# Performance work log

Hardware: AMD Instinct MI355X
Metric: run time of the kernel (lower is better)

Reference implementation:

```python
import jax, jax.numpy as jnp
import numpy as np

EPS = 1e-5
NEG_SLOPE = 0.2  # GATConv default negative_slope


def layer_norm(x, g, b):
    mu = jnp.mean(x, axis=-1, keepdims=True)
    var = jnp.mean((x - mu) ** 2, axis=-1, keepdims=True)
    return (x - mu) * jax.lax.rsqrt(var + EPS) * g + b


def setup_inputs() -> dict:
    key = jax.random.key(0)
    ks = jax.random.split(key, 16)
    B, NPG = 64, 1024          # graphs, fine nodes per graph
    NF = B * NPG               # 65536 fine nodes
    IN, HID, ATT, H, LLM = 1024, 1024, 64, 8, 2048
    D = ATT * H                # 512
    w = lambda k, shp: (jax.random.normal(k, shp, jnp.float32) * 0.02)
    # structured bipartite star edges: fine node i -> global node i // NPG
    edge_index = jnp.stack([jnp.arange(NF, dtype=jnp.int32),
                            (jnp.arange(NF, dtype=jnp.int32) // NPG)])
    return {
        "x_fine": jax.random.normal(ks[0], (NF, IN), jnp.float32),
        "x_global": jax.random.normal(ks[1], (B, D), jnp.float32),
        "edge_index_fine_global": edge_index,
        "nf_g": jnp.ones((IN,), jnp.float32), "nf_b": jnp.zeros((IN,), jnp.float32),
        "ip_w1": w(ks[2], (IN, HID)), "ip_b1": jnp.zeros((HID,), jnp.float32),
        "ip_w2": w(ks[3], (HID, D)), "ip_b2": jnp.zeros((D,), jnp.float32),
        "ng_g": jnp.ones((D,), jnp.float32), "ng_b": jnp.zeros((D,), jnp.float32),
        "gat_ws": w(ks[4], (D, D)), "gat_wd": w(ks[5], (D, D)),
        "att_s": w(ks[6], (1, H, ATT)), "att_d": w(ks[7], (1, H, ATT)),
        "gat_bias": jnp.zeros((D,), jnp.float32),
        "gp_w": w(ks[8], (D, LLM)), "gp_b": jnp.zeros((LLM,), jnp.float32),
        "fp_w": w(ks[9], (D, LLM)), "fp_b": jnp.zeros((LLM,), jnp.float32),
    }


def reference(x_fine, x_global, edge_index_fine_global,
              nf_g, nf_b, ip_w1, ip_b1, ip_w2, ip_b2, ng_g, ng_b,
              gat_ws, gat_wd, att_s, att_d, gat_bias,
              gp_w, gp_b, fp_w, fp_b):
    B = x_global.shape[0]
    H = att_s.shape[1]
    C = x_global.shape[1] // H

    # fine branch: LayerNorm -> MLP projection to H*C
    xf = layer_norm(x_fine, nf_g, nf_b)
    xf = jax.nn.relu(xf @ ip_w1 + ip_b1) @ ip_w2 + ip_b2      # [NF, H*C]
    xg = layer_norm(x_global, ng_g, ng_b)                      # [B, H*C]

    # bipartite GATConv (eval mode: attention dropout disabled)
    xs = (xf @ gat_ws).reshape(-1, H, C)                       # [NF, H, C]
    xd = (xg @ gat_wd).reshape(B, H, C)                        # [B, H, C]
    a_s = jnp.sum(xs * att_s, axis=-1)                         # [NF, H]
    a_d = jnp.sum(xd * att_d, axis=-1)                         # [B, H]

    row, col = edge_index_fine_global[0], edge_index_fine_global[1]
    loops = jnp.arange(B, dtype=row.dtype)                     # add_self_loops: nodes < min(NF,B)
    rows = jnp.concatenate([row, loops])
    cols = jnp.concatenate([col, loops])
    # PyG removes pre-existing self-loop edges; emulate by masking them out
    self_mask = jnp.concatenate([row == col, jnp.zeros((B,), bool)])

    logits = jax.nn.leaky_relu(a_s[rows] + a_d[cols], NEG_SLOPE)   # [E+B, H]
    logits = jnp.where(self_mask[:, None], -jnp.inf, logits)
    m = jax.ops.segment_max(logits, cols, num_segments=B)         # [B, H]
    e = jnp.exp(logits - m[cols])
    e = jnp.where(self_mask[:, None], 0.0, e)
    denom = jax.ops.segment_sum(e, cols, num_segments=B)
    alpha = e / denom[cols]                                       # [E+B, H]

    msg = xs[rows] * alpha[..., None]                              # [E+B, H, C]
    agg = jax.ops.segment_sum(msg, cols, num_segments=B)          # [B, H, C]
    xg = agg.reshape(B, H * C) + gat_bias + xg                    # GAT out + residual

    og = (xg @ gp_w + gp_b)[:, None, :]                            # [B, 1, LLM]
    of = (xf @ fp_w + fp_b).reshape(B, -1, fp_w.shape[1])          # [B, NPG, LLM]
    return jnp.concatenate([og, of], axis=1)                       # [B, 1+NPG, LLM]
```

## Files before the change

### kernel.cpp

```cpp
#include <hip/hip_runtime.h>
#include <hip/hip_bf16.h>
#include <math.h>

typedef __bf16 bf16_t;
typedef bf16_t bf16x8 __attribute__((ext_vector_type(8)));
typedef bf16_t bf16x4 __attribute__((ext_vector_type(4)));
typedef float f32x4 __attribute__((ext_vector_type(4)));

#define DEVINL __device__ __forceinline__

DEVINL float wave_reduce_sum(float v) {
#pragma unroll
  for (int o = 32; o > 0; o >>= 1) v += __shfl_down(v, o);
  return v;
}
DEVINL float block_reduce_sum256(float v, float* red) {
  int tid = threadIdx.x;
  __syncthreads();
  v = wave_reduce_sum(v);
  if ((tid & 63) == 0) red[tid >> 6] = v;
  __syncthreads();
  return red[0] + red[1] + red[2] + red[3];
}

__global__ __launch_bounds__(256) void k_ln_fine(const float* __restrict__ x,
                                                 const float* __restrict__ g,
                                                 const float* __restrict__ b,
                                                 bf16_t* __restrict__ out) {
  constexpr int CPT = 4, COLS = 1024;
  __shared__ float red[8];
  const size_t row = blockIdx.x;
  const float* xr = x + row * COLS;
  const int c0 = threadIdx.x * CPT;
  float v[CPT];
#pragma unroll
  for (int j = 0; j < CPT; j++) v[j] = xr[c0 + j];
  float s = 0;
#pragma unroll
  for (int j = 0; j < CPT; j++) s += v[j];
  const float mu = block_reduce_sum256(s, red) * (1.0f / COLS);
  float q = 0;
#pragma unroll
  for (int j = 0; j < CPT; j++) { float d = v[j] - mu; q += d * d; }
  const float var = block_reduce_sum256(q, red) * (1.0f / COLS);
  const float rs = rsqrtf(var + 1e-5f);
  bf16x4 o;
#pragma unroll
  for (int j = 0; j < CPT; j++)
    o[j] = (bf16_t)((v[j] - mu) * rs * g[c0 + j] + b[c0 + j]);
  *(bf16x4*)(out + row * COLS + c0) = o;
}

__global__ __launch_bounds__(256) void k_prep(
    const float* __restrict__ ip_w1, const float* __restrict__ ip_w2,
    const float* __restrict__ fp_w, const float* __restrict__ gat_wd,
    const float* __restrict__ att_d, const float* __restrict__ gat_ws,
    const float* __restrict__ att_s, const float* __restrict__ x_global,
    const float* __restrict__ ng_g, const float* __restrict__ ng_b,
    bf16_t* __restrict__ w1t, bf16_t* __restrict__ w2t, bf16_t* __restrict__ fpt,
    float* __restrict__ wd_att, float* __restrict__ wsatt, float* __restrict__ xg) {
  __shared__ float t[32][33];
  __shared__ float red[8];
  const int bid = blockIdx.x, tid = threadIdx.x;
  if (bid < 2560) {
    const float* src;
    bf16_t* dst;
    int N, n0, k0;
    if (bid < 1024) {
      src = ip_w1; dst = w1t; N = 1024;
      n0 = (bid & 31) * 32; k0 = (bid >> 5) * 32;
    } else if (bid < 1536) {
      const int rel = bid - 1024;
      src = ip_w2; dst = w2t; N = 512;
      n0 = (rel & 15) * 32; k0 = (rel >> 4) * 32;
    } else {
      const int rel = bid - 1536;
      src = fp_w; dst = fpt; N = 2048;
      n0 = (rel & 63) * 32; k0 = (rel >> 6) * 32;
    }
    const int K = (bid < 1536) ? 1024 : 512;
    const int tx = tid & 31, ty = tid >> 5;
#pragma unroll
    for (int i = 0; i < 32; i += 8)
      t[ty + i][tx] = src[(size_t)(k0 + ty + i) * N + n0 + tx];
    __syncthreads();
#pragma unroll
    for (int i = 0; i < 32; i += 8)
      dst[(size_t)(n0 + ty + i) * K + k0 + tx] = (bf16_t)t[tx][ty + i];
  } else if (bid < 2564) {
    const int rel = bid - 2560;
    const float* W = (rel < 2) ? gat_wd : gat_ws;
    const float* att = (rel < 2) ? att_d : att_s;
    float* outp = (rel < 2) ? wd_att : wsatt;
    const int k = (rel & 1) * 256 + tid;
#pragma unroll
    for (int h = 0; h < 8; h++) {
      float s = 0;
      for (int c = 0; c < 64; c++)
        s += W[(size_t)k * 512 + h * 64 + c] * att[h * 64 + c];
      outp[k * 8 + h] = s;
    }
  } else {
    const int row = bid - 2564;
    const float* xr = x_global + (size_t)row * 512;
    const int c0 = tid * 2;
    float v0 = xr[c0], v1 = xr[c0 + 1];
    const float mu = block_reduce_sum256(v0 + v1, red) * (1.0f / 512);
    const float d0 = v0 - mu, d1 = v1 - mu;
    const float var = block_reduce_sum256(d0 * d0 + d1 * d1, red) * (1.0f / 512);
    const float rs = rsqrtf(var + 1e-5f);
    xg[(size_t)row * 512 + c0] = d0 * rs * ng_g[c0] + ng_b[c0];
    xg[(size_t)row * 512 + c0 + 1] = d1 * rs * ng_g[c0 + 1] + ng_b[c0 + 1];
  }
}

template <int N, int K, int EPI>
__global__ __launch_bounds__(256, 2) void gemm_bt(const bf16_t* __restrict__ A,
                                                  const bf16_t* __restrict__ Bt,
                                                  const float* __restrict__ bias,
                                                  void* __restrict__ Cout) {
  __shared__ bf16_t As[128 * 64];
  __shared__ bf16_t Bs[128 * 64];
  const int tid = threadIdx.x;
  const int lane = tid & 63;
  const int wid = tid >> 6;
  const int wm = wid >> 1, wn = wid & 1;
  const size_t arow0 = (size_t)blockIdx.x * 128;
  const int bcol0 = blockIdx.y * 128;

  f32x4 acc[4][4] = {};
  const int kTiles = K / 64;
  for (int kt = 0; kt < kTiles; ++kt) {
    const int k0 = kt * 64;
#pragma unroll
    for (int i = 0; i < 4; ++i) {
      const int c = i * 256 + tid;
      const int r = c >> 3, kc = (c & 7) * 8;
      const bf16_t* ga = A + (arow0 + r) * K + k0 + kc;
      __builtin_amdgcn_global_load_lds(
          (const __attribute__((address_space(1))) void*)ga,
          (__attribute__((address_space(3))) void*)(As + c * 8), 16, 0, 0);
      const bf16_t* gb = Bt + ((size_t)bcol0 + r) * K + k0 + kc;
      __builtin_amdgcn_global_load_lds(
          (const __attribute__((address_space(1))) void*)gb,
          (__attribute__((address_space(3))) void*)(Bs + c * 8), 16, 0, 0);
    }
    __syncthreads();
#pragma unroll
    for (int kk = 0; kk < 2; ++kk) {
      bf16x8 af[4], bfr[4];
      const int kofs = kk * 32 + (lane >> 4) * 8;
#pragma unroll
      for (int m = 0; m < 4; ++m)
        af[m] = *(const bf16x8*)(As + (wm * 64 + m * 16 + (lane & 15)) * 64 + kofs);
#pragma unroll
      for (int n = 0; n < 4; ++n)
        bfr[n] = *(const bf16x8*)(Bs + (wn * 64 + n * 16 + (lane & 15)) * 64 + kofs);
#pragma unroll
      for (int m = 0; m < 4; ++m)
#pragma unroll
        for (int n = 0; n < 4; ++n)
          acc[m][n] = __builtin_amdgcn_mfma_f32_16x16x32_bf16(af[m], bfr[n], acc[m][n], 0, 0, 0);
    }
    __syncthreads();
  }
  const int lr = (lane >> 4) * 4;
  const int lc = lane & 15;
#pragma unroll
  for (int n = 0; n < 4; ++n) {
    const int col = bcol0 + wn * 64 + n * 16 + lc;
    const float bv = bias[col];
#pragma unroll
    for (int m = 0; m < 4; ++m) {
#pragma unroll
      for (int j = 0; j < 4; ++j) {
        const size_t row = arow0 + wm * 64 + m * 16 + lr + j;
        float v = acc[m][n][j] + bv;
        if constexpr (EPI == 0) v = v > 0.0f ? v : 0.0f;
        if constexpr (EPI == 3) {
          const size_t orow = row + (row >> 10) + 1;
          ((float*)Cout)[orow * (size_t)N + col] = v;
        } else {
          ((bf16_t*)Cout)[row * (size_t)N + col] = (bf16_t)v;
        }
      }
    }
  }
}

__global__ __launch_bounds__(256) void k_as(const bf16_t* __restrict__ xf,
                                            const float* __restrict__ wsatt,
                                            float* __restrict__ a_s) {
  const int tid = threadIdx.x, l = tid & 63, wid = tid >> 6;
  float wreg[64];
#pragma unroll
  for (int q = 0; q < 16; q++) {
    const float4 v = *(const float4*)(wsatt + l * 64 + q * 4);
    wreg[q * 4 + 0] = v.x; wreg[q * 4 + 1] = v.y;
    wreg[q * 4 + 2] = v.z; wreg[q * 4 + 3] = v.w;
  }
  const size_t base = (size_t)blockIdx.x * 128 + wid * 32;
  for (int rr = 0; rr < 32; rr++) {
    const size_t i = base + rr;
    const bf16x8 v = *(const bf16x8*)(xf + i * 512 + l * 8);
    float p[8] = {};
#pragma unroll
    for (int u = 0; u < 8; u++) {
      const float xv = (float)v[u];
#pragma unroll
      for (int h = 0; h < 8; h++) p[h] += xv * wreg[u * 8 + h];
    }
#pragma unroll
    for (int h = 0; h < 8; h++)
#pragma unroll
      for (int mk = 1; mk < 64; mk <<= 1) p[h] += __shfl_xor(p[h], mk);
    float outv = 0.0f;
#pragma unroll
    for (int h = 0; h < 8; h++) outv = (l == h) ? p[h] : outv;
    if (l < 8) a_s[i * 8 + l] = outv;
  }
}

__global__ __launch_bounds__(512) void k_alpha_z(const float* __restrict__ a_s,
                                                 const bf16_t* __restrict__ xf,
                                                 const float* __restrict__ xg,
                                                 const float* __restrict__ wd_att,
                                                 float* __restrict__ zq) {
  __shared__ float sal[8][260];
  const int b = blockIdx.x >> 2, qq = blockIdx.x & 3;
  const int tid = threadIdx.x, l = tid & 63, h = tid >> 6;
  float pa = 0;
#pragma unroll
  for (int u = 0; u < 8; u++)
    pa += xg[b * 512 + l * 8 + u] * wd_att[(l * 8 + u) * 8 + h];
#pragma unroll
  for (int mk = 1; mk < 64; mk <<= 1) pa += __shfl_xor(pa, mk);
  const float ad = pa;
  const float* asb = a_s + (size_t)b * 1024 * 8;
  float lg[16];
  float lmax = -1e30f;
#pragma unroll
  for (int j = 0; j < 16; j++) {
    const float a = asb[(l + j * 64) * 8 + h] + ad;
    lg[j] = a > 0.0f ? a : 0.2f * a;
    lmax = fmaxf(lmax, lg[j]);
  }
  float lself = -INFINITY;
  if (l == 0 && b != 0) {
    const float a = a_s[b * 8 + h] + ad;
    lself = a > 0.0f ? a : 0.2f * a;
  }
  lmax = fmaxf(lmax, lself);
#pragma unroll
  for (int mk = 1; mk < 64; mk <<= 1) lmax = fmaxf(lmax, __shfl_xor(lmax, mk));
  float ps = 0;
#pragma unroll
  for (int j = 0; j < 16; j++) { lg[j] = __expf(lg[j] - lmax); ps += lg[j]; }
  const float eself = (l == 0 && lself != -INFINITY) ? __expf(lself - lmax) : 0.0f;
  ps += eself;
#pragma unroll
  for (int mk = 1; mk < 64; mk <<= 1) ps += __shfl_xor(ps, mk);
  const float inv = 1.0f / ps;
#pragma unroll
  for (int j = 0; j < 4; j++) sal[h][l + j * 64] = lg[qq * 4 + j] * inv;
  if (l == 0) sal[h][256] = (qq == 0) ? eself * inv : 0.0f;
  __syncthreads();
  float zp[8] = {};
  const bf16_t* xb = xf + ((size_t)b * 1024 + qq * 256) * 512 + l * 8;
  for (int i = 0; i < 256; i += 2) {
    const float a0 = sal[h][i], a1 = sal[h][i + 1];
    const bf16x8 v0 = *(const bf16x8*)(xb + (size_t)i * 512);
    const bf16x8 v1 = *(const bf16x8*)(xb + (size_t)(i + 1) * 512);
#pragma unroll
    for (int u = 0; u < 8; u++) zp[u] += a0 * (float)v0[u] + a1 * (float)v1[u];
  }
  if (qq == 0) {
    const float a = sal[h][256];
    const bf16x8 v = *(const bf16x8*)(xf + (size_t)b * 512 + l * 8);
#pragma unroll
    for (int u = 0; u < 8; u++) zp[u] += a * (float)v[u];
  }
  float4 o0 = {zp[0], zp[1], zp[2], zp[3]};
  float4 o1 = {zp[4], zp[5], zp[6], zp[7]};
  float* zo = zq + (((size_t)b * 4 + qq) * 8 + h) * 512 + l * 8;
  *(float4*)zo = o0;
  *(float4*)(zo + 4) = o1;
}

__global__ __launch_bounds__(512) void k_fin(const float* __restrict__ zq,
                                             const float* __restrict__ ws,
                                             const float* __restrict__ gat_bias,
                                             const float* __restrict__ xg,
                                             float* __restrict__ aggx) {
  __shared__ float zsum[4096];
  const int b = blockIdx.x, c = threadIdx.x, h = c >> 6;
  const float* zb = zq + (size_t)b * 4 * 4096;
  for (int idx = c; idx < 4096; idx += 512)
    zsum[idx] = zb[idx] + zb[4096 + idx] + zb[8192 + idx] + zb[12288 + idx];
  __syncthreads();
  const float* zr = zsum + h * 512;
  float acc = 0;
#pragma unroll 8
  for (int k = 0; k < 512; k++) acc += zr[k] * ws[(size_t)k * 512 + c];
  aggx[b * 512 + c] = acc + gat_bias[c] + xg[b * 512 + c];
}

__global__ __launch_bounds__(256) void k_og(const float* __restrict__ aggx,
                                            const float* __restrict__ gp_w,
                                            const float* __restrict__ gp_b,
                                            float* __restrict__ out) {
  __shared__ float xv[512];
  const int b = blockIdx.y;
  const int c = blockIdx.x * 256 + threadIdx.x;
  for (int k = threadIdx.x; k < 512; k += 256) xv[k] = aggx[b * 512 + k];
  __syncthreads();
  float acc = gp_b[c];
#pragma unroll 8
  for (int k = 0; k < 512; k++) acc += xv[k] * gp_w[(size_t)k * 2048 + c];
  out[(size_t)b * 1025 * 2048 + c] = acc;
}

extern "C" void kernel_launch(void* const* d_in, const int* in_sizes, int n_in,
                              void* d_out, int out_size, void* d_ws, size_t ws_size,
                              hipStream_t stream) {
  const float* x_fine   = (const float*)d_in[0];
  const float* x_global = (const float*)d_in[1];
  const float* nf_g  = (const float*)d_in[3];
  const float* nf_b  = (const float*)d_in[4];
  const float* ip_w1 = (const float*)d_in[5];
  const float* ip_b1 = (const float*)d_in[6];
  const float* ip_w2 = (const float*)d_in[7];
  const float* ip_b2 = (const float*)d_in[8];
  const float* ng_g  = (const float*)d_in[9];
  const float* ng_b  = (const float*)d_in[10];
  const float* gat_ws   = (const float*)d_in[11];
  const float* gat_wd   = (const float*)d_in[12];
  const float* att_s    = (const float*)d_in[13];
  const float* att_d    = (const float*)d_in[14];
  const float* gat_bias = (const float*)d_in[15];
  const float* gp_w = (const float*)d_in[16];
  const float* gp_b = (const float*)d_in[17];
  const float* fp_w = (const float*)d_in[18];
  const float* fp_b = (const float*)d_in[19];
  float* out = (float*)d_out;

  char* ws = (char*)d_ws;
  bf16_t* xf_ln = (bf16_t*)ws;
  bf16_t* hbuf  = (bf16_t*)(ws + 134217728ULL);
  char* sm = ws + 268435456ULL;
  bf16_t* w1t  = (bf16_t*)sm;
  bf16_t* w2t  = (bf16_t*)(sm + 2097152ULL);
  bf16_t* fpt  = (bf16_t*)(sm + 3145728ULL);
  float*  a_s  = (float*)(sm + 5242880ULL);
  float*  xg   = (float*)(sm + 7340032ULL);
  float*  wd_att = (float*)(sm + 7471104ULL);
  float*  wsatt  = (float*)(sm + 7487488ULL);
  float*  zbuf4  = (float*)(sm + 7503872ULL);
  float*  aggx   = (float*)(sm + 11698176ULL);
  bf16_t* xf = xf_ln;

  k_prep<<<2628, 256, 0, stream>>>(ip_w1, ip_w2, fp_w, gat_wd, att_d, gat_ws,
                                   att_s, x_global, ng_g, ng_b, w1t, w2t, fpt,
                                   wd_att, wsatt, xg);

  k_ln_fine<<<65536, 256, 0, stream>>>(x_fine, nf_g, nf_b, xf_ln);

  gemm_bt<1024, 1024, 0><<<dim3(512, 8), 256, 0, stream>>>(xf_ln, w1t, ip_b1, hbuf);
  gemm_bt<512, 1024, 1><<<dim3(512, 4), 256, 0, stream>>>(hbuf, w2t, ip_b2, xf);

  k_as<<<512, 256, 0, stream>>>(xf, wsatt, a_s);
  k_alpha_z<<<256, 512, 0, stream>>>(a_s, xf, xg, wd_att, zbuf4);
  k_fin<<<64, 512, 0, stream>>>(zbuf4, gat_ws, gat_bias, xg, aggx);
  k_og<<<dim3(8, 64), 256, 0, stream>>>(aggx, gp_w, gp_b, out);

  gemm_bt<2048, 512, 3><<<dim3(512, 16), 256, 0, stream>>>(xf, fpt, fp_b, out);
}
```

Baseline: 812.1 us.

## Transpose MFMA operands for vectorized GEMM epilogue stores and fuse GAT finish with output projection

The GEMM swaps the MFMA operand order so each lane holds four consecutive output columns of one row. The epilogue can then load the bias as a float4 and write float4 (fp32) or bf16x4 stores instead of scattered scalar stores. This matters most for the large fp32 output GEMM, which writes about 537 MB. Separately, the k_fin and k_og kernels are fused into one kernel that keeps aggx in shared memory, and the min-blocks-per-CU launch bound of 2 is removed. The fused kernel runs only 64 blocks for the gp_w product, so that small stage has less parallelism.

New measurement: 944.5 us. +16.3%, slower.

```diff
diff --git a/kernel.cpp b/kernel.cpp
--- a/kernel.cpp
+++ b/kernel.cpp
@@ -115,10 +115,10 @@
 }
 
 template <int N, int K, int EPI>
-__global__ __launch_bounds__(256, 2) void gemm_bt(const bf16_t* __restrict__ A,
-                                                  const bf16_t* __restrict__ Bt,
-                                                  const float* __restrict__ bias,
-                                                  void* __restrict__ Cout) {
+__global__ __launch_bounds__(256) void gemm_bt(const bf16_t* __restrict__ A,
+                                               const bf16_t* __restrict__ Bt,
+                                               const float* __restrict__ bias,
+                                               void* __restrict__ Cout) {
   __shared__ bf16_t As[128 * 64];
   __shared__ bf16_t Bs[128 * 64];
   const int tid = threadIdx.x;
@@ -160,29 +160,34 @@
       for (int m = 0; m < 4; ++m)
 #pragma unroll
         for (int n = 0; n < 4; ++n)
-          acc[m][n] = __builtin_amdgcn_mfma_f32_16x16x32_bf16(af[m], bfr[n], acc[m][n], 0, 0, 0);
+          acc[n][m] = __builtin_amdgcn_mfma_f32_16x16x32_bf16(bfr[n], af[m], acc[n][m], 0, 0, 0);
     }
     __syncthreads();
   }
-  const int lr = (lane >> 4) * 4;
+  const int lr4 = (lane >> 4) * 4;
   const int lc = lane & 15;
 #pragma unroll
   for (int n = 0; n < 4; ++n) {
-    const int col = bcol0 + wn * 64 + n * 16 + lc;
-    const float bv = bias[col];
+    const int col0 = bcol0 + wn * 64 + n * 16 + lr4;
+    const float4 bvv = *(const float4*)(bias + col0);
 #pragma unroll
     for (int m = 0; m < 4; ++m) {
+      const size_t row = arow0 + wm * 64 + m * 16 + lc;
+      float v[4];
 #pragma unroll
       for (int j = 0; j < 4; ++j) {
-        const size_t row = arow0 + wm * 64 + m * 16 + lr + j;
-        float v = acc[m][n][j] + bv;
-        if constexpr (EPI == 0) v = v > 0.0f ? v : 0.0f;
-        if constexpr (EPI == 3) {
-          const size_t orow = row + (row >> 10) + 1;
-          ((float*)Cout)[orow * (size_t)N + col] = v;
-        } else {
-          ((bf16_t*)Cout)[row * (size_t)N + col] = (bf16_t)v;
-        }
+        v[j] = acc[n][m][j] + ((const float*)&bvv)[j];
+        if constexpr (EPI == 0) v[j] = v[j] > 0.0f ? v[j] : 0.0f;
+      }
+      if constexpr (EPI == 3) {
+        const size_t orow = row + (row >> 10) + 1;
+        float4 o = {v[0], v[1], v[2], v[3]};
+        *(float4*)((float*)Cout + orow * (size_t)N + col0) = o;
+      } else {
+        bf16x4 o;
+#pragma unroll
+        for (int j = 0; j < 4; ++j) o[j] = (bf16_t)v[j];
+        *(bf16x4*)((bf16_t*)Cout + row * (size_t)N + col0) = o;
       }
     }
   }
@@ -287,12 +292,15 @@
   *(float4*)(zo + 4) = o1;
 }
 
-__global__ __launch_bounds__(512) void k_fin(const float* __restrict__ zq,
-                                             const float* __restrict__ ws,
-                                             const float* __restrict__ gat_bias,
-                                             const float* __restrict__ xg,
-                                             float* __restrict__ aggx) {
+__global__ __launch_bounds__(512) void k_finog(const float* __restrict__ zq,
+                                               const float* __restrict__ ws,
+                                               const float* __restrict__ gat_bias,
+                                               const float* __restrict__ xg,
+                                               const float* __restrict__ gp_w,
+                                               const float* __restrict__ gp_b,
+                                               float* __restrict__ out) {
   __shared__ float zsum[4096];
+  __shared__ float aggx[512];
   const int b = blockIdx.x, c = threadIdx.x, h = c >> 6;
   const float* zb = zq + (size_t)b * 4 * 4096;
   for (int idx = c; idx < 4096; idx += 512)
@@ -302,22 +310,16 @@
   float acc = 0;
 #pragma unroll 8
   for (int k = 0; k < 512; k++) acc += zr[k] * ws[(size_t)k * 512 + c];
-  aggx[b * 512 + c] = acc + gat_bias[c] + xg[b * 512 + c];
-}
-
-__global__ __launch_bounds__(256) void k_og(const float* __restrict__ aggx,
-                                            const float* __restrict__ gp_w,
-                                            const float* __restrict__ gp_b,
-                                            float* __restrict__ out) {
-  __shared__ float xv[512];
-  const int b = blockIdx.y;
-  const int c = blockIdx.x * 256 + threadIdx.x;
-  for (int k = threadIdx.x; k < 512; k += 256) xv[k] = aggx[b * 512 + k];
-  __syncthreads();
-  float acc = gp_b[c];
+  aggx[c] = acc + gat_bias[c] + xg[b * 512 + c];
+  __syncthreads();
+#pragma unroll
+  for (int j = 0; j < 4; j++) {
+    const int cc = c + j * 512;
+    float o = gp_b[cc];
 #pragma unroll 8
-  for (int k = 0; k < 512; k++) acc += xv[k] * gp_w[(size_t)k * 2048 + c];
-  out[(size_t)b * 1025 * 2048 + c] = acc;
+    for (int k = 0; k < 512; k++) o += aggx[k] * gp_w[(size_t)k * 2048 + cc];
+    out[(size_t)b * 1025 * 2048 + cc] = o;
+  }
 }
 
 extern "C" void kernel_launch(void* const* d_in, const int* in_sizes, int n_in,
@@ -356,7 +358,6 @@
   float*  wd_att = (float*)(sm + 7471104ULL);
   float*  wsatt  = (float*)(sm + 7487488ULL);
   float*  zbuf4  = (float*)(sm + 7503872ULL);
-  float*  aggx   = (float*)(sm + 11698176ULL);
   bf16_t* xf = xf_ln;
 
   k_prep<<<2628, 256, 0, stream>>>(ip_w1, ip_w2, fp_w, gat_wd, att_d, gat_ws,
@@ -370,8 +371,7 @@
 
   k_as<<<512, 256, 0, stream>>>(xf, wsatt, a_s);
   k_alpha_z<<<256, 512, 0, stream>>>(a_s, xf, xg, wd_att, zbuf4);
-  k_fin<<<64, 512, 0, stream>>>(zbuf4, gat_ws, gat_bias, xg, aggx);
-  k_og<<<dim3(8, 64), 256, 0, stream>>>(aggx, gp_w, gp_b, out);
+  k_finog<<<64, 512, 0, stream>>>(zbuf4, gat_ws, gat_bias, xg, gp_w, gp_b, out);
 
   gemm_bt<2048, 512, 3><<<dim3(512, 16), 256, 0, stream>>>(xf, fpt, fp_b, out);
 }
```
